# Kernel optimization log

Hardware: AMD Instinct MI355X
Metric: run time of the kernel (lower is better)

The kernel has to match this reference:

```python
import jax, jax.numpy as jnp
import numpy as np

B, N, C, H = 8, 4096, 256, 8
D = C // H
HID = 4 * C
EPS = 1e-5

def _ln(x, w, b):
    mu = jnp.mean(x, axis=-1, keepdims=True)
    var = jnp.var(x, axis=-1, keepdims=True)
    return (x - mu) * jax.lax.rsqrt(var + EPS) * w + b

def setup_inputs() -> dict:
    key = jax.random.key(0)
    ks = jax.random.split(key, 16)
    s = lambda k, shp, scale=0.02: jax.random.normal(k, shp, dtype=jnp.float32) * scale
    return {
        "input_": jax.random.normal(ks[0], (B, N, C), dtype=jnp.float32),
        "prev_state": jax.random.normal(ks[1], (B, N, C), dtype=jnp.float32),
        "pos_embed": jax.random.normal(ks[2], (1, N, C), dtype=jnp.float32),
        "norm1_w": jnp.ones((C,), jnp.float32), "norm1_b": jnp.zeros((C,), jnp.float32),
        "norm2_w": jnp.ones((C,), jnp.float32), "norm2_b": jnp.zeros((C,), jnp.float32),
        "norm3_w": jnp.ones((C,), jnp.float32), "norm3_b": jnp.zeros((C,), jnp.float32),
        "qkv_input_w": s(ks[3], (3 * C, C)),
        "qkv_state_w": s(ks[4], (3 * C, C)),
        "proj_w": s(ks[5], (C, C)), "proj_b": jnp.zeros((C,), jnp.float32),
        "gate_w": s(ks[6], (C, 2 * C)), "gate_b": jnp.zeros((C,), jnp.float32),
        "fc1_w": s(ks[7], (HID, C)), "fc1_b": jnp.zeros((HID,), jnp.float32),
        "fc2_w": s(ks[8], (C, HID)), "fc2_b": jnp.zeros((C,), jnp.float32),
    }

def reference(input_, prev_state, pos_embed,
              norm1_w, norm1_b, norm2_w, norm2_b, norm3_w, norm3_b,
              qkv_input_w, qkv_state_w, proj_w, proj_b,
              gate_w, gate_b, fc1_w, fc1_b, fc2_w, fc2_b):
    input_pos = input_ + pos_embed
    x_ln = _ln(input_pos, norm1_w, norm1_b)
    s_ln = _ln(prev_state, norm2_w, norm2_b)
    # fused QKV from input and state; torch Linear: x @ W.T
    qkv_i = (x_ln @ qkv_input_w.T).reshape(B, N, 3, H, D).transpose(2, 0, 3, 1, 4)
    qkv_s = (s_ln @ qkv_state_w.T).reshape(B, N, 3, H, D).transpose(2, 0, 3, 1, 4)
    q = qkv_i[0] + qkv_s[0]  # [B,H,N,D]
    k = qkv_i[1] + qkv_s[1]
    v = qkv_i[2] + qkv_s[2]
    phi_q = jax.nn.elu(q) + 1.0
    phi_k = jax.nn.elu(k) + 1.0
    # (phi_q @ phi_k^T) @ v reordered associatively to O(N*D^2)
    kv = jnp.einsum('bhnd,bhne->bhde', phi_k, v)        # [B,H,D,D]
    attn = jnp.einsum('bhnd,bhde->bhne', phi_q, kv)     # [B,H,N,D]
    attn = attn.transpose(0, 2, 1, 3).reshape(B, N, C)
    attn = attn @ proj_w.T + proj_b
    output = input_pos + attn
    stacked = jnp.concatenate([input_, prev_state], axis=2)
    update = jax.nn.sigmoid(stacked @ gate_w.T + gate_b)
    new_state = prev_state * (1.0 - update) + attn * update
    h = _ln(output, norm3_w, norm3_b)
    h = jax.nn.gelu(h @ fc1_w.T + fc1_b, approximate=False) @ fc2_w.T + fc2_b
    output = output + h
    return (output, new_state)
```

## Files before the change

### kernel.cpp

```cpp
#include <hip/hip_runtime.h>
#include <cmath>

typedef unsigned short u16;
typedef __attribute__((ext_vector_type(8))) short short8;
typedef __attribute__((ext_vector_type(4))) float f32x4;
typedef __attribute__((ext_vector_type(4))) u16 u16x4;

__device__ __forceinline__ float b2f(u16 u) {
    unsigned x = ((unsigned)u) << 16;
    return __builtin_bit_cast(float, x);
}
__device__ __forceinline__ u16 f2b(float f) {
    unsigned x = __builtin_bit_cast(unsigned, f);
    unsigned r = (x + 0x7fffu + ((x >> 16) & 1u)) >> 16;
    return (u16)r;
}
__device__ __forceinline__ float loadx(const void* p, size_t i, int f32) {
    return f32 ? ((const float*)p)[i] : b2f(((const u16*)p)[i]);
}
__device__ __forceinline__ void storex(void* p, size_t i, float v, int f32) {
    if (f32) ((float*)p)[i] = v; else ((u16*)p)[i] = f2b(v);
}
__device__ __forceinline__ void stage8f(u16* dst, const void* src, size_t eoff) {
    const f32x4* s = (const f32x4*)((const float*)src + eoff);
    f32x4 a = s[0], b = s[1];
    uint4 p;
    p.x = (unsigned)f2b(a[0]) | ((unsigned)f2b(a[1]) << 16);
    p.y = (unsigned)f2b(a[2]) | ((unsigned)f2b(a[3]) << 16);
    p.z = (unsigned)f2b(b[0]) | ((unsigned)f2b(b[1]) << 16);
    p.w = (unsigned)f2b(b[2]) | ((unsigned)f2b(b[3]) << 16);
    *(uint4*)dst = p;
}
__device__ __forceinline__ void gl_lds16(const void* g, void* l) {
    __builtin_amdgcn_global_load_lds(
        (const __attribute__((address_space(1))) void*)g,
        (__attribute__((address_space(3))) void*)l, 16, 0, 0);
}

#define BB 8
#define NN 4096
#define CC 256
#define HH 8
#define DD 32
#define HID 1024
#define MTOK (BB*NN)
#define TOKEL ((size_t)MTOK*CC)

#define WS_INPUT_POS 0u
#define WS_PHIQ   16777216u
#define WS_PHIK   33554432u
#define WS_V      50331648u
#define WS_XLN    67108864u
#define WS_SLN    83886080u
#define WS_OUTPRE 100663296u
#define WS_FLAG   117440512u

__global__ __launch_bounds__(64) void detect_kernel(const u16* __restrict__ in0,
                                                    int* __restrict__ flag)
{
    int t = threadIdx.x;
    u16 w = in0[2 * t];
    int e = (w >> 7) & 0xFF;
    int bad = (e < 64 || e > 192) ? 1 : 0;
    unsigned long long m = __ballot(bad);
    if (t == 0) *flag = (__popcll(m) > 8) ? 1 : 0;
}

__global__ __launch_bounds__(256) void prep_kernel(
    const void* __restrict__ inp, const void* __restrict__ prev,
    const void* __restrict__ pos,
    const void* __restrict__ w1, const void* __restrict__ b1,
    const void* __restrict__ w2, const void* __restrict__ b2,
    u16* __restrict__ input_pos, u16* __restrict__ x_ln, u16* __restrict__ s_ln,
    const int* __restrict__ flagp)
{
    const int f32 = *flagp;
    const int m = blockIdx.x;
    const int c = threadIdx.x;
    const int n = m & (NN - 1);
    const size_t idx = (size_t)m * CC + c;

    __shared__ float red[8];

    float ip = loadx(inp, idx, f32) + loadx(pos, (size_t)n * CC + c, f32);
    float s = ip, s2 = ip * ip;
    #pragma unroll
    for (int o = 32; o; o >>= 1) { s += __shfl_down(s, o, 64); s2 += __shfl_down(s2, o, 64); }
    if ((threadIdx.x & 63) == 0) { int w6 = threadIdx.x >> 6; red[w6] = s; red[4 + w6] = s2; }
    __syncthreads();
    float mu  = (red[0] + red[1] + red[2] + red[3]) * (1.f / 256.f);
    float var = (red[4] + red[5] + red[6] + red[7]) * (1.f / 256.f) - mu * mu;
    float rs = rsqrtf(var + 1e-5f);
    input_pos[idx] = f2b(ip);
    x_ln[idx] = f2b((ip - mu) * rs * loadx(w1, c, f32) + loadx(b1, c, f32));
    __syncthreads();

    float pv = loadx(prev, idx, f32);
    s = pv; s2 = pv * pv;
    #pragma unroll
    for (int o = 32; o; o >>= 1) { s += __shfl_down(s, o, 64); s2 += __shfl_down(s2, o, 64); }
    if ((threadIdx.x & 63) == 0) { int w6 = threadIdx.x >> 6; red[w6] = s; red[4 + w6] = s2; }
    __syncthreads();
    mu  = (red[0] + red[1] + red[2] + red[3]) * (1.f / 256.f);
    var = (red[4] + red[5] + red[6] + red[7]) * (1.f / 256.f) - mu * mu;
    rs = rsqrtf(var + 1e-5f);
    s_ln[idx] = f2b((pv - mu) * rs * loadx(w2, c, f32) + loadx(b2, c, f32));
}

__global__ __launch_bounds__(256) void ln3_kernel(
    const u16* __restrict__ op, const void* __restrict__ w,
    const void* __restrict__ b, u16* __restrict__ out, const int* __restrict__ flagp)
{
    const int f32 = *flagp;
    const size_t m = blockIdx.x;
    const int c = threadIdx.x;
    const size_t idx = m * CC + c;
    __shared__ float red[8];
    float x = b2f(op[idx]);
    float s = x, s2 = x * x;
    #pragma unroll
    for (int o = 32; o; o >>= 1) { s += __shfl_down(s, o, 64); s2 += __shfl_down(s2, o, 64); }
    if ((threadIdx.x & 63) == 0) { int w6 = threadIdx.x >> 6; red[w6] = s; red[4 + w6] = s2; }
    __syncthreads();
    float mu  = (red[0] + red[1] + red[2] + red[3]) * (1.f / 256.f);
    float var = (red[4] + red[5] + red[6] + red[7]) * (1.f / 256.f) - mu * mu;
    out[idx] = f2b((x - mu) * rsqrtf(var + 1e-5f) * loadx(w, c, f32) + loadx(b, c, f32));
}

__global__ __launch_bounds__(64) void kv_mfma(
    const u16* __restrict__ phik_t, const u16* __restrict__ v_t,
    float* __restrict__ kvout)
{
    const int bh = blockIdx.x;
    const int k0 = blockIdx.y * 256;
    const int lane = threadIdx.x;
    const int quad = lane >> 4, lr = lane & 15;

    const u16* A = phik_t + (size_t)bh * DD * NN;
    const u16* W = v_t    + (size_t)bh * DD * NN;

    f32x4 acc[2][2];
    #pragma unroll
    for (int i = 0; i < 2; ++i)
        #pragma unroll
        for (int j = 0; j < 2; ++j) { f32x4 z = {0.f,0.f,0.f,0.f}; acc[i][j] = z; }

    for (int kk = k0; kk < k0 + 256; kk += 32) {
        short8 a0 = *(const short8*)(A + (size_t)lr * NN + kk + quad * 8);
        short8 a1 = *(const short8*)(A + (size_t)(16 + lr) * NN + kk + quad * 8);
        short8 w0 = *(const short8*)(W + (size_t)lr * NN + kk + quad * 8);
        short8 w1 = *(const short8*)(W + (size_t)(16 + lr) * NN + kk + quad * 8);
        acc[0][0] = __builtin_amdgcn_mfma_f32_16x16x32_bf16(a0, w0, acc[0][0], 0, 0, 0);
        acc[0][1] = __builtin_amdgcn_mfma_f32_16x16x32_bf16(a0, w1, acc[0][1], 0, 0, 0);
        acc[1][0] = __builtin_amdgcn_mfma_f32_16x16x32_bf16(a1, w0, acc[1][0], 0, 0, 0);
        acc[1][1] = __builtin_amdgcn_mfma_f32_16x16x32_bf16(a1, w1, acc[1][1], 0, 0, 0);
    }
    float* base = kvout + (size_t)bh * (DD * DD);
    #pragma unroll
    for (int i = 0; i < 2; ++i)
        #pragma unroll
        for (int j = 0; j < 2; ++j)
            #pragma unroll
            for (int r = 0; r < 4; ++r)
                atomicAdd(base + (i * 16 + quad * 4 + r) * DD + j * 16 + lr, acc[i][j][r]);
}

__global__ __launch_bounds__(256) void attn_mfma(
    const u16* __restrict__ phiq, const float* __restrict__ kv,
    u16* __restrict__ attn_tok)
{
    const int bh = blockIdx.x;
    const int b = bh >> 3, h = bh & 7;
    const int wv = threadIdx.x >> 6, lane = threadIdx.x & 63;
    const int quad = lane >> 4, lr = lane & 15;

    const float* kvb = kv + (size_t)bh * (DD * DD);
    short8 bf0, bf1;
    #pragma unroll
    for (int j = 0; j < 8; ++j) {
        int d = quad * 8 + j;
        bf0[j] = (short)f2b(kvb[d * DD + lr]);
        bf1[j] = (short)f2b(kvb[d * DD + 16 + lr]);
    }

    const u16* qb = phiq + (size_t)bh * NN * DD;
    const int n0 = blockIdx.y * 512 + wv * 128;
    #pragma unroll
    for (int t = 0; t < 8; ++t) {
        const int nt = n0 + t * 16;
        short8 af = *(const short8*)(qb + (size_t)(nt + lr) * DD + quad * 8);
        f32x4 c0 = {0.f,0.f,0.f,0.f}, c1 = {0.f,0.f,0.f,0.f};
        c0 = __builtin_amdgcn_mfma_f32_16x16x32_bf16(af, bf0, c0, 0, 0, 0);
        c1 = __builtin_amdgcn_mfma_f32_16x16x32_bf16(af, bf1, c1, 0, 0, 0);
        size_t base = ((size_t)b * NN + nt + quad * 4) * CC + h * DD;
        #pragma unroll
        for (int r = 0; r < 4; ++r) {
            attn_tok[base + (size_t)r * CC + lr]      = f2b(c0[r]);
            attn_tok[base + (size_t)r * CC + 16 + lr] = f2b(c1[r]);
        }
    }
}

#define BM 128
#define BN 128
#define BK 32
#define LDT 32

template <int MODE, int RAWA>
__global__ __launch_bounds__(256) void gemm_bt(
    const void* __restrict__ A1, const void* __restrict__ A2,
    const void* __restrict__ W1, const void* __restrict__ W2,
    int lda, int ldw, int K, int Ksplit, int wcol2,
    const void* __restrict__ bias,
    u16* __restrict__ o0, u16* __restrict__ o1,
    const u16* __restrict__ xa, const void* __restrict__ xr,
    void* __restrict__ oraw, const int* __restrict__ flagp)
{
    __shared__ u16 ash[BM * LDT];
    __shared__ u16 bsh[BN * LDT];

    const int f32 = *flagp;
    const int af32 = RAWA ? f32 : 0;

    const int tid = threadIdx.x;
    const int lane = tid & 63;
    const int wv = tid >> 6;
    const int wm = wv >> 1, wn = wv & 1;
    const int quad = lane >> 4, lr = lane & 15;

    f32x4 acc[4][4];
    #pragma unroll
    for (int i = 0; i < 4; ++i)
        #pragma unroll
        for (int j = 0; j < 4; ++j) { f32x4 z = {0.f,0.f,0.f,0.f}; acc[i][j] = z; }

    const size_t arow0 = (size_t)blockIdx.y * BM;
    const size_t wrow0 = (size_t)blockIdx.x * BN;

    const int srow = lane >> 2;
    const int skc  = (lane & 3) << 3;

    for (int k0 = 0; k0 < K; k0 += BK) {
        const void* As; const void* Ws; int ka, kw;
        if (k0 < Ksplit) { As = A1; Ws = W1; ka = k0;          kw = k0; }
        else             { As = A2; Ws = W2; ka = k0 - Ksplit; kw = k0 - Ksplit + wcol2; }

        if (!af32) {
            const u16* ga = (const u16*)As + (arow0 + wv * 32 + srow) * (size_t)lda + ka + skc;
            u16* la = ash + (wv * 32) * LDT;
            gl_lds16(ga, la);
            gl_lds16(ga + (size_t)16 * lda, la + 16 * LDT);
        } else {
            #pragma unroll
            for (int half = 0; half < 2; ++half) {
                int row = wv * 32 + half * 16 + srow;
                stage8f(ash + row * LDT + skc, As, (arow0 + row) * (size_t)lda + ka + skc);
            }
        }
        if (!f32) {
            const u16* gw = (const u16*)Ws + (wrow0 + wv * 32 + srow) * (size_t)ldw + kw + skc;
            u16* lb = bsh + (wv * 32) * LDT;
            gl_lds16(gw, lb);
            gl_lds16(gw + (size_t)16 * ldw, lb + 16 * LDT);
        } else {
            #pragma unroll
            for (int half = 0; half < 2; ++half) {
                int row = wv * 32 + half * 16 + srow;
                stage8f(bsh + row * LDT + skc, Ws, (wrow0 + row) * (size_t)ldw + kw + skc);
            }
        }
        __syncthreads();

        short8 af[4], bf[4];
        #pragma unroll
        for (int i = 0; i < 4; ++i)
            af[i] = *(const short8*)(ash + (wm * 64 + i * 16 + lr) * LDT + quad * 8);
        #pragma unroll
        for (int j = 0; j < 4; ++j)
            bf[j] = *(const short8*)(bsh + (wn * 64 + j * 16 + lr) * LDT + quad * 8);
        #pragma unroll
        for (int i = 0; i < 4; ++i)
            #pragma unroll
            for (int j = 0; j < 4; ++j)
                acc[i][j] = __builtin_amdgcn_mfma_f32_16x16x32_bf16(af[i], bf[j], acc[i][j], 0, 0, 0);
        __syncthreads();
    }

    const int mbase = blockIdx.y * BM + wm * 64;
    const int nbase = blockIdx.x * BN + wn * 64;
    #pragma unroll
    for (int i = 0; i < 4; ++i) {
        #pragma unroll
        for (int j = 0; j < 4; ++j) {
            if (MODE == 0) {
                const int c = nbase + j * 16 + lr;
                const int which = c >> 8, rem = c & 255, h = rem >> 5, d = rem & 31;
                const int m0 = mbase + i * 16 + quad * 4;
                const int b = m0 >> 12, n0i = m0 & (NN - 1);
                if (which == 0) {
                    size_t base = (((size_t)b * HH + h) * NN + n0i) * DD + d;
                    #pragma unroll
                    for (int r = 0; r < 4; ++r) {
                        float v = acc[i][j][r];
                        v = (v > 0.f) ? (v + 1.f) : expf(v);
                        o0[base + (size_t)r * DD] = f2b(v);
                    }
                } else {
                    u16x4 p;
                    #pragma unroll
                    for (int r = 0; r < 4; ++r) {
                        float v = acc[i][j][r];
                        if (which == 1) v = (v > 0.f) ? (v + 1.f) : expf(v);
                        p[r] = f2b(v);
                    }
                    u16* dst = o0 + (size_t)which * TOKEL;
                    *(u16x4*)(dst + (((size_t)b * HH + h) * DD + d) * NN + n0i) = p;
                }
            } else {
                #pragma unroll
                for (int r = 0; r < 4; ++r) {
                    int m = mbase + i * 16 + quad * 4 + r;
                    int c = nbase + j * 16 + lr;
                    float v = acc[i][j][r];
                    if (MODE == 1) {
                        float val = v + loadx(bias, c, f32);
                        size_t idx = (size_t)m * CC + c;
                        o1[idx] = f2b(b2f(xa[idx]) + val);
                        o0[idx] = f2b(val);
                    } else if (MODE == 2) {
                        float u = 1.f / (1.f + expf(-(v + loadx(bias, c, f32))));
                        size_t idx = (size_t)m * CC + c;
                        float ap = b2f(xa[idx]);
                        float pv = loadx(xr, idx, f32);
                        storex(oraw, TOKEL + idx, pv * (1.f - u) + ap * u, f32);
                    } else if (MODE == 3) {
                        float x = v + loadx(bias, c, f32);
                        float g = 0.5f * x * (1.f + erff(x * 0.70710678118654752f));
                        o0[(size_t)m * HID + c] = f2b(g);
                    } else {
                        float val = v + loadx(bias, c, f32);
                        size_t idx = (size_t)m * CC + c;
                        storex(oraw, idx, b2f(xa[idx]) + val, f32);
                    }
                }
            }
        }
    }
}

extern "C" void kernel_launch(void* const* d_in, const int* in_sizes, int n_in,
                              void* d_out, int out_size, void* d_ws, size_t ws_size,
                              hipStream_t stream)
{
    const void* input_ = d_in[0];
    const void* prev   = d_in[1];
    const void* pos    = d_in[2];
    const void* n1w = d_in[3];  const void* n1b = d_in[4];
    const void* n2w = d_in[5];  const void* n2b = d_in[6];
    const void* n3w = d_in[7];  const void* n3b = d_in[8];
    const void* qkvi = d_in[9]; const void* qkvs = d_in[10];
    const void* projw = d_in[11]; const void* projb = d_in[12];
    const void* gatew = d_in[13]; const void* gateb = d_in[14];
    const void* fc1w = d_in[15]; const void* fc1b = d_in[16];
    const void* fc2w = d_in[17]; const void* fc2b = d_in[18];

    char* ws = (char*)d_ws;
    u16* input_pos = (u16*)(ws + WS_INPUT_POS);
    u16* phiq  = (u16*)(ws + WS_PHIQ);
    u16* phikt = (u16*)(ws + WS_PHIK);
    u16* vt    = (u16*)(ws + WS_V);
    u16* x_ln = (u16*)(ws + WS_XLN);
    u16* s_ln = (u16*)(ws + WS_SLN);
    u16* attn_tok = x_ln;
    u16* attn_proj = phikt;
    float* kvf = (float*)(ws + WS_SLN);
    u16* ln3o = s_ln;
    u16* outpre = (u16*)(ws + WS_OUTPRE);
    u16* h1 = (u16*)(ws + WS_INPUT_POS);
    int* flagp = (int*)(ws + WS_FLAG);

    detect_kernel<<<1, 64, 0, stream>>>((const u16*)input_, flagp);
    prep_kernel<<<MTOK, 256, 0, stream>>>(input_, prev, pos, n1w, n1b, n2w, n2b,
                                          input_pos, x_ln, s_ln, flagp);
    gemm_bt<0, 0><<<dim3(3 * CC / BN, MTOK / BM), 256, 0, stream>>>(
        x_ln, s_ln, qkvi, qkvs, CC, CC, 2 * CC, CC, 0, nullptr,
        phiq, nullptr, nullptr, nullptr, nullptr, flagp);
    hipMemsetAsync((void*)kvf, 0, BB * HH * DD * DD * sizeof(float), stream);
    kv_mfma<<<dim3(BB * HH, 16), 64, 0, stream>>>(phikt, vt, kvf);
    attn_mfma<<<dim3(BB * HH, NN / 512), 256, 0, stream>>>(phiq, kvf, attn_tok);
    gemm_bt<1, 0><<<dim3(CC / BN, MTOK / BM), 256, 0, stream>>>(
        attn_tok, attn_tok, projw, projw, CC, CC, CC, CC, 0, projb,
        attn_proj, outpre, input_pos, nullptr, nullptr, flagp);
    gemm_bt<2, 1><<<dim3(CC / BN, MTOK / BM), 256, 0, stream>>>(
        input_, prev, gatew, gatew, CC, 2 * CC, 2 * CC, CC, CC, gateb,
        nullptr, nullptr, attn_proj, prev, d_out, flagp);
    ln3_kernel<<<MTOK, 256, 0, stream>>>(outpre, n3w, n3b, ln3o, flagp);
    gemm_bt<3, 0><<<dim3(HID / BN, MTOK / BM), 256, 0, stream>>>(
        ln3o, ln3o, fc1w, fc1w, CC, CC, CC, CC, 0, fc1b,
        h1, nullptr, nullptr, nullptr, nullptr, flagp);
    gemm_bt<4, 0><<<dim3(CC / BN, MTOK / BM), 256, 0, stream>>>(
        h1, h1, fc2w, fc2w, HID, HID, HID, HID, 0, fc2b,
        nullptr, nullptr, outpre, nullptr, d_out, flagp);
}
```

Before: 527.1 us.

## Swap MFMA operands to transpose accumulator layout for vectorized epilogue stores

Swaps the A/B operands of the MFMA in the GEMM kernel for the non-QKV modes and for the Q block columns of the QKV GEMM. Each lane then holds four consecutive output columns of one row, so the epilogues can load bias and residuals and store outputs as 4-wide vectors instead of scattered scalar accesses. It also replaces the exact erf GELU with a tanh approximation and uses fast __expf. The aim is to cut global memory transactions and transcendental cost in the epilogues, at the risk of small numerical differences from the GELU approximation.

```diff
diff --git a/kernel.cpp b/kernel.cpp
--- a/kernel.cpp
+++ b/kernel.cpp
@@ -17,9 +17,6 @@
 }
 __device__ __forceinline__ float loadx(const void* p, size_t i, int f32) {
     return f32 ? ((const float*)p)[i] : b2f(((const u16*)p)[i]);
-}
-__device__ __forceinline__ void storex(void* p, size_t i, float v, int f32) {
-    if (f32) ((float*)p)[i] = v; else ((u16*)p)[i] = f2b(v);
 }
 __device__ __forceinline__ void stage8f(u16* dst, const void* src, size_t eoff) {
     const f32x4* s = (const f32x4*)((const float*)src + eoff);
@@ -35,6 +32,12 @@
     __builtin_amdgcn_global_load_lds(
         (const __attribute__((address_space(1))) void*)g,
         (__attribute__((address_space(3))) void*)l, 16, 0, 0);
+}
+__device__ __forceinline__ float gelu_f(float x) {
+    float y = 0.7978845608028654f * (x + 0.044715f * x * x * x);
+    float e = __expf(2.f * y);
+    float t = 1.f - 2.f / (e + 1.f);
+    return 0.5f * x * (1.f + t);
 }
 
 #define BB 8
@@ -227,6 +230,8 @@
     const int wv = tid >> 6;
     const int wm = wv >> 1, wn = wv & 1;
     const int quad = lane >> 4, lr = lane & 15;
+
+    const bool swp = (MODE == 0) ? (blockIdx.x < 2) : true;
 
     f32x4 acc[4][4];
     #pragma unroll
@@ -278,69 +283,125 @@
         #pragma unroll
         for (int j = 0; j < 4; ++j)
             bf[j] = *(const short8*)(bsh + (wn * 64 + j * 16 + lr) * LDT + quad * 8);
-        #pragma unroll
-        for (int i = 0; i < 4; ++i)
+        if (swp) {
             #pragma unroll
-            for (int j = 0; j < 4; ++j)
-                acc[i][j] = __builtin_amdgcn_mfma_f32_16x16x32_bf16(af[i], bf[j], acc[i][j], 0, 0, 0);
+            for (int i = 0; i < 4; ++i)
+                #pragma unroll
+                for (int j = 0; j < 4; ++j)
+                    acc[i][j] = __builtin_amdgcn_mfma_f32_16x16x32_bf16(bf[j], af[i], acc[i][j], 0, 0, 0);
+        } else {
+            #pragma unroll
+            for (int i = 0; i < 4; ++i)
+                #pragma unroll
+                for (int j = 0; j < 4; ++j)
+                    acc[i][j] = __builtin_amdgcn_mfma_f32_16x16x32_bf16(af[i], bf[j], acc[i][j], 0, 0, 0);
+        }
         __syncthreads();
     }
 
     const int mbase = blockIdx.y * BM + wm * 64;
     const int nbase = blockIdx.x * BN + wn * 64;
+    constexpr int LDOUT = (MODE == 3) ? HID : CC;
+
     #pragma unroll
     for (int i = 0; i < 4; ++i) {
         #pragma unroll
         for (int j = 0; j < 4; ++j) {
             if (MODE == 0) {
-                const int c = nbase + j * 16 + lr;
-                const int which = c >> 8, rem = c & 255, h = rem >> 5, d = rem & 31;
-                const int m0 = mbase + i * 16 + quad * 4;
-                const int b = m0 >> 12, n0i = m0 & (NN - 1);
-                if (which == 0) {
-                    size_t base = (((size_t)b * HH + h) * NN + n0i) * DD + d;
+                if (swp) {
+                    const int m = mbase + i * 16 + lr;
+                    const int b = m >> 12, n = m & (NN - 1);
+                    const int c0 = nbase + j * 16 + quad * 4;
+                    const int h = c0 >> 5, d0 = c0 & 31;
+                    u16x4 p;
                     #pragma unroll
                     for (int r = 0; r < 4; ++r) {
                         float v = acc[i][j][r];
-                        v = (v > 0.f) ? (v + 1.f) : expf(v);
-                        o0[base + (size_t)r * DD] = f2b(v);
+                        p[r] = f2b((v > 0.f) ? (v + 1.f) : __expf(v));
                     }
+                    *(u16x4*)(o0 + (((size_t)b * HH + h) * NN + n) * DD + d0) = p;
                 } else {
+                    const int c = nbase + j * 16 + lr;
+                    const int which = c >> 8, rem = c & 255, h = rem >> 5, d = rem & 31;
+                    const int m0 = mbase + i * 16 + quad * 4;
+                    const int b = m0 >> 12, n0i = m0 & (NN - 1);
                     u16x4 p;
                     #pragma unroll
                     for (int r = 0; r < 4; ++r) {
                         float v = acc[i][j][r];
-                        if (which == 1) v = (v > 0.f) ? (v + 1.f) : expf(v);
+                        if (which == 1) v = (v > 0.f) ? (v + 1.f) : __expf(v);
                         p[r] = f2b(v);
                     }
                     u16* dst = o0 + (size_t)which * TOKEL;
                     *(u16x4*)(dst + (((size_t)b * HH + h) * DD + d) * NN + n0i) = p;
                 }
             } else {
-                #pragma unroll
-                for (int r = 0; r < 4; ++r) {
-                    int m = mbase + i * 16 + quad * 4 + r;
-                    int c = nbase + j * 16 + lr;
-                    float v = acc[i][j][r];
-                    if (MODE == 1) {
-                        float val = v + loadx(bias, c, f32);
-                        size_t idx = (size_t)m * CC + c;
-                        o1[idx] = f2b(b2f(xa[idx]) + val);
-                        o0[idx] = f2b(val);
-                    } else if (MODE == 2) {
-                        float u = 1.f / (1.f + expf(-(v + loadx(bias, c, f32))));
-                        size_t idx = (size_t)m * CC + c;
-                        float ap = b2f(xa[idx]);
-                        float pv = loadx(xr, idx, f32);
-                        storex(oraw, TOKEL + idx, pv * (1.f - u) + ap * u, f32);
-                    } else if (MODE == 3) {
-                        float x = v + loadx(bias, c, f32);
-                        float g = 0.5f * x * (1.f + erff(x * 0.70710678118654752f));
-                        o0[(size_t)m * HID + c] = f2b(g);
+                const int m = mbase + i * 16 + lr;
+                const int c0 = nbase + j * 16 + quad * 4;
+                const size_t idx0 = (size_t)m * LDOUT + c0;
+                float bias4[4];
+                if (f32) {
+                    f32x4 t = *(const f32x4*)((const float*)bias + c0);
+                    #pragma unroll
+                    for (int r = 0; r < 4; ++r) bias4[r] = t[r];
+                } else {
+                    u16x4 t = *(const u16x4*)((const u16*)bias + c0);
+                    #pragma unroll
+                    for (int r = 0; r < 4; ++r) bias4[r] = b2f(t[r]);
+                }
+                if (MODE == 1) {
+                    u16x4 xa4 = *(const u16x4*)(xa + idx0);
+                    u16x4 po, pr;
+                    #pragma unroll
+                    for (int r = 0; r < 4; ++r) {
+                        float val = acc[i][j][r] + bias4[r];
+                        po[r] = f2b(val);
+                        pr[r] = f2b(b2f(xa4[r]) + val);
+                    }
+                    *(u16x4*)(o0 + idx0) = po;
+                    *(u16x4*)(o1 + idx0) = pr;
+                } else if (MODE == 2) {
+                    u16x4 ap4 = *(const u16x4*)(xa + idx0);
+                    float res[4];
+                    if (f32) {
+                        f32x4 pv = *(const f32x4*)((const float*)xr + idx0);
+                        #pragma unroll
+                        for (int r = 0; r < 4; ++r) {
+                            float u = 1.f / (1.f + __expf(-(acc[i][j][r] + bias4[r])));
+                            res[r] = pv[r] * (1.f - u) + b2f(ap4[r]) * u;
+                        }
+                        f32x4 o; o[0]=res[0]; o[1]=res[1]; o[2]=res[2]; o[3]=res[3];
+                        *(f32x4*)((float*)oraw + TOKEL + idx0) = o;
                     } else {
-                        float val = v + loadx(bias, c, f32);
-                        size_t idx = (size_t)m * CC + c;
-                        storex(oraw, idx, b2f(xa[idx]) + val, f32);
+                        u16x4 pv = *(const u16x4*)((const u16*)xr + idx0);
+                        u16x4 o;
+                        #pragma unroll
+                        for (int r = 0; r < 4; ++r) {
+                            float u = 1.f / (1.f + __expf(-(acc[i][j][r] + bias4[r])));
+                            o[r] = f2b(b2f(pv[r]) * (1.f - u) + b2f(ap4[r]) * u);
+                        }
+                        *(u16x4*)((u16*)oraw + TOKEL + idx0) = o;
+                    }
+                } else if (MODE == 3) {
+                    u16x4 p;
+                    #pragma unroll
+                    for (int r = 0; r < 4; ++r)
+                        p[r] = f2b(gelu_f(acc[i][j][r] + bias4[r]));
+                    *(u16x4*)(o0 + idx0) = p;
+                } else {
+                    u16x4 xa4 = *(const u16x4*)(xa + idx0);
+                    if (f32) {
+                        f32x4 o;
+                        #pragma unroll
+                        for (int r = 0; r < 4; ++r)
+                            o[r] = b2f(xa4[r]) + acc[i][j][r] + bias4[r];
+                        *(f32x4*)((float*)oraw + idx0) = o;
+                    } else {
+                        u16x4 o;
+                        #pragma unroll
+                        for (int r = 0; r < 4; ++r)
+                            o[r] = f2b(b2f(xa4[r]) + acc[i][j][r] + bias4[r]);
+                        *(u16x4*)((u16*)oraw + idx0) = o;
                     }
                 }
             }
```

Result: faster. 506.4 us (-3.9%).
